# Kernel optimization log

Hardware: AMD Instinct MI355X
Metric: run time of the kernel (lower is better)

Reference implementation:

```python
import jax, jax.numpy as jnp
import numpy as np

B, T, H, V, S = 64, 32, 512, 32000, 400


def setup_inputs() -> dict:
    key = jax.random.key(0)
    ks = jax.random.split(key, 14)
    f = lambda k, s: jax.random.normal(k, s, dtype=jnp.float32)
    return {
        "inputs": jax.random.randint(ks[0], (B, T), 0, V),
        "embedding0": f(ks[1], (B, H)),
        "output0": f(ks[2], (B, H)),
        "tree_h0": f(ks[3], (B, H)),
        "tree_c0": f(ks[4], (B, H)),
        "tree_context": f(ks[5], (B, S, H)),
        "text_h0": f(ks[6], (B, H)),
        "text_c0": f(ks[7], (B, H)),
        "text_context": f(ks[8], (B, S, H)),
        "word_emb": f(ks[9], (V, H)) * 0.02,
        "Wx": f(ks[10], (2 * H, 4 * H)) * 0.02,   # LSTM input weights (input_size = 2H)
        "Wh": f(ks[11], (H, 4 * H)) * 0.02,       # LSTM recurrent weights
        "b": jnp.zeros((4 * H,), jnp.float32),
        "W_in": f(ks[12], (H, H)) * 0.02,         # attention score projection
        "W_out": f(ks[13], (4 * H, H)) * 0.02,    # attention combine projection
    }


def _lstm_cell(x, h, c, Wx, Wh, b):
    g = x @ Wx + h @ Wh + b                      # [B,4H]
    i, f, gg, o = jnp.split(g, 4, axis=-1)
    c_new = jax.nn.sigmoid(f) * c + jax.nn.sigmoid(i) * jnp.tanh(gg)
    h_new = jax.nn.sigmoid(o) * jnp.tanh(c_new)
    return h_new, c_new


def _attend(h, ctx, W_in):
    target = h @ W_in                             # [B,H]
    scores = jnp.einsum('bsh,bh->bs', ctx, target)
    attn = jax.nn.softmax(scores, axis=-1)
    return jnp.einsum('bs,bsh->bh', attn, ctx)    # weighted context [B,H]


def reference(inputs, embedding0, output0, tree_h0, tree_c0, tree_context,
              text_h0, text_c0, text_context, word_emb, Wx, Wh, b, W_in, W_out):
    embeddings = word_emb[inputs]                 # [B,T,H]
    embeddings = jnp.transpose(embeddings, (1, 0, 2))  # time-major [T,B,H]

    def step(carry, emb_i):
        emb, out, th, tc, xh, xc = carry
        x = jnp.concatenate([emb, out], axis=1)   # [B,2H]
        th, tc = _lstm_cell(x, th, tc, Wx, Wh, b)  # tree branch (shared weights)
        xh, xc = _lstm_cell(x, xh, xc, Wx, Wh, b)  # text branch (shared weights)
        w_tree = _attend(th, tree_context, W_in)
        w_text = _attend(xh, text_context, W_in)
        combined = jnp.concatenate([w_tree, w_text, th, xh], axis=1)  # [B,4H]
        out = jnp.tanh(combined @ W_out)           # dropout = identity (eval mode)
        return (emb_i, out, th, tc, xh, xc), out

    carry0 = (embedding0, output0, tree_h0, tree_c0, text_h0, text_c0)
    _, outs = jax.lax.scan(step, carry0, embeddings)  # outs: [T,B,H]
    return jnp.transpose(outs, (1, 0, 2))             # [B,T,H]
```

## Files before the change

### kernel.cpp

```cpp
#include <hip/hip_runtime.h>
#include <hip/hip_bf16.h>
#include <math.h>

#define BB 64
#define TT 32
#define HH 512
#define H2 1024
#define H4 2048
#define SS 400

#define OFF_WT_HI 0u
#define OFF_WT_LO 1572864u
#define OFF_WIT_HI 3145728u
#define OFF_WIT_LO 3276800u
#define OFF_EH    3407872u
#define OFF_EL    3932160u
#define OFF_OH    4456448u
#define OFF_OL    4472832u
#define OFF_HHP   4489216u
#define OFF_HLP   4521984u
#define OFF_TC    4554752u
#define OFF_XC    4620288u
#define OFF_TH    4685824u
#define OFF_XH    4751360u
#define OFF_G     4816896u
#define OFF_TGTP  6914048u
#define OFF_PACC  7438336u
#define OFF_PML   7962624u
#define OFF_CTX16 7964672u
#define WS_NEED_F 21071872u
#define OFF_WOT_HI 21071872u
#define OFF_WOT_LO 21596160u
#define OFF_COMBH  22120448u
#define OFF_COMBL  22153216u
#define WS_NEED2_F 22185984u
#define OFF_PART  OFF_G

typedef short bf16x8 __attribute__((ext_vector_type(8)));
typedef float f32x4  __attribute__((ext_vector_type(4)));

__device__ __forceinline__ float sigm(float x){ return 1.f/(1.f+__expf(-x)); }

__device__ __forceinline__ unsigned short bf_rn(float x){
  unsigned int u = __float_as_uint(x);
  return (unsigned short)((u + 0x7fffu + ((u>>16)&1u)) >> 16);
}
__device__ __forceinline__ void split2(float x, unsigned short &h, unsigned short &l){
  h = bf_rn(x);
  float hf = __uint_as_float(((unsigned int)h)<<16);
  l = bf_rn(x - hf);
}
__device__ __forceinline__ float blo(unsigned int u){ return __uint_as_float(u<<16); }
__device__ __forceinline__ float bhi(unsigned int u){ return __uint_as_float(u & 0xffff0000u); }

__global__ __launch_bounds__(256) void k_wprep(const float* __restrict__ Wx,
    const float* __restrict__ Wh, unsigned short* __restrict__ wt_hi,
    unsigned short* __restrict__ wt_lo){
  __shared__ float lds[64][68];
  int bk = blockIdx.x >> 5, bn = blockIdx.x & 31;
  int k0 = bk*64, n0 = bn*64;
  int tid = threadIdx.x;
  #pragma unroll
  for (int i=0;i<4;i++){
    int flat = tid + i*256;
    int k = flat >> 4, nq = flat & 15;
    int kg = k0 + k;
    const float* srow = (kg < 1024) ? Wx + (size_t)kg*H4 : Wh + (size_t)(kg-1024)*H4;
    float4 v = *(const float4*)(srow + n0 + nq*4);
    *(float4*)&lds[k][nq*4] = v;
  }
  __syncthreads();
  #pragma unroll
  for (int i=0;i<2;i++){
    int flat = tid + i*256;
    int n = flat >> 3, k8 = flat & 7;
    ushort4 h0, h1, l0, l1;
    unsigned short h[8], l[8];
    #pragma unroll
    for (int j=0;j<8;j++) split2(lds[k8*8+j][n], h[j], l[j]);
    h0.x=h[0];h0.y=h[1];h0.z=h[2];h0.w=h[3]; h1.x=h[4];h1.y=h[5];h1.z=h[6];h1.w=h[7];
    l0.x=l[0];l0.y=l[1];l0.z=l[2];l0.w=l[3]; l1.x=l[4];l1.y=l[5];l1.z=l[6];l1.w=l[7];
    size_t dst = (size_t)(n0+n)*1536 + k0 + k8*8;
    *(ushort4*)(wt_hi+dst) = h0; *(ushort4*)(wt_hi+dst+4) = h1;
    *(ushort4*)(wt_lo+dst) = l0; *(ushort4*)(wt_lo+dst+4) = l1;
  }
}

__global__ __launch_bounds__(256) void k_wiprep(const float* __restrict__ W_in,
    unsigned short* __restrict__ wit_hi, unsigned short* __restrict__ wit_lo){
  __shared__ float lds[64][68];
  int bk = blockIdx.x >> 3, bn = blockIdx.x & 7;
  int k0 = bk*64, n0 = bn*64;
  int tid = threadIdx.x;
  #pragma unroll
  for (int i=0;i<4;i++){
    int flat = tid + i*256;
    int k = flat >> 4, nq = flat & 15;
    float4 v = *(const float4*)(W_in + (size_t)(k0+k)*HH + n0 + nq*4);
    *(float4*)&lds[k][nq*4] = v;
  }
  __syncthreads();
  #pragma unroll
  for (int i=0;i<2;i++){
    int flat = tid + i*256;
    int n = flat >> 3, k8 = flat & 7;
    ushort4 h0, h1, l0, l1;
    unsigned short h[8], l[8];
    #pragma unroll
    for (int j=0;j<8;j++) split2(lds[k8*8+j][n], h[j], l[j]);
    h0.x=h[0];h0.y=h[1];h0.z=h[2];h0.w=h[3]; h1.x=h[4];h1.y=h[5];h1.z=h[6];h1.w=h[7];
    l0.x=l[0];l0.y=l[1];l0.z=l[2];l0.w=l[3]; l1.x=l[4];l1.y=l[5];l1.z=l[6];l1.w=l[7];
    size_t dst = (size_t)(n0+n)*HH + k0 + k8*8;
    *(ushort4*)(wit_hi+dst) = h0; *(ushort4*)(wit_hi+dst+4) = h1;
    *(ushort4*)(wit_lo+dst) = l0; *(ushort4*)(wit_lo+dst+4) = l1;
  }
}

__global__ __launch_bounds__(256) void k_woprep(const float* __restrict__ W_out,
    unsigned short* __restrict__ wot_hi, unsigned short* __restrict__ wot_lo){
  __shared__ float lds[64][68];
  int bk = blockIdx.x >> 3, bn = blockIdx.x & 7;
  int k0 = bk*64, n0 = bn*64;
  int tid = threadIdx.x;
  #pragma unroll
  for (int i=0;i<4;i++){
    int flat = tid + i*256;
    int k = flat >> 4, nq = flat & 15;
    float4 v = *(const float4*)(W_out + (size_t)(k0+k)*HH + n0 + nq*4);
    *(float4*)&lds[k][nq*4] = v;
  }
  __syncthreads();
  #pragma unroll
  for (int i=0;i<2;i++){
    int flat = tid + i*256;
    int n = flat >> 3, k8 = flat & 7;
    ushort4 h0, h1, l0, l1;
    unsigned short h[8], l[8];
    #pragma unroll
    for (int j=0;j<8;j++) split2(lds[k8*8+j][n], h[j], l[j]);
    h0.x=h[0];h0.y=h[1];h0.z=h[2];h0.w=h[3]; h1.x=h[4];h1.y=h[5];h1.z=h[6];h1.w=h[7];
    l0.x=l[0];l0.y=l[1];l0.z=l[2];l0.w=l[3]; l1.x=l[4];l1.y=l[5];l1.z=l[6];l1.w=l[7];
    size_t dst = (size_t)(n0+n)*H4 + k0 + k8*8;
    *(ushort4*)(wot_hi+dst) = h0; *(ushort4*)(wot_hi+dst+4) = h1;
    *(ushort4*)(wot_lo+dst) = l0; *(ushort4*)(wot_lo+dst+4) = l1;
  }
}

__global__ __launch_bounds__(256) void k_ctx16(const float* __restrict__ src,
    unsigned short* __restrict__ dst){
  size_t off = ((size_t)blockIdx.x*256 + threadIdx.x)*8;
  float4 a = *(const float4*)(src + off);
  float4 c = *(const float4*)(src + off + 4);
  ushort4 u0, u1;
  u0.x=bf_rn(a.x); u0.y=bf_rn(a.y); u0.z=bf_rn(a.z); u0.w=bf_rn(a.w);
  u1.x=bf_rn(c.x); u1.y=bf_rn(c.y); u1.z=bf_rn(c.z); u1.w=bf_rn(c.w);
  *(ushort4*)(dst+off) = u0;
  *(ushort4*)(dst+off+4) = u1;
}

__global__ __launch_bounds__(128) void k_prep(const int* __restrict__ inp,
    const float* __restrict__ emb0, const float* __restrict__ wemb,
    unsigned short* __restrict__ eh, unsigned short* __restrict__ el){
  int n = blockIdx.x; int t = n >> 6, b = n & 63;
  const float* src = (t==0) ? emb0 + (size_t)b*HH
                            : wemb + (size_t)inp[b*TT + (t-1)]*HH;
  float4 v = ((const float4*)src)[threadIdx.x];
  ushort4 h, l;
  split2(v.x,h.x,l.x); split2(v.y,h.y,l.y); split2(v.z,h.z,l.z); split2(v.w,h.w,l.w);
  size_t base = ((size_t)t*BB + b)*HH + threadIdx.x*4;
  *(ushort4*)(eh+base) = h; *(ushort4*)(el+base) = l;
}

__global__ __launch_bounds__(256) void k_init(const float* __restrict__ th0,
    const float* __restrict__ tc0, const float* __restrict__ xh0,
    const float* __restrict__ xc0, const float* __restrict__ out0,
    float* __restrict__ ws){
  unsigned short* hhp = (unsigned short*)(ws + OFF_HHP);
  unsigned short* hlp = (unsigned short*)(ws + OFF_HLP);
  unsigned short* oh  = (unsigned short*)(ws + OFF_OH);
  unsigned short* ol  = (unsigned short*)(ws + OFF_OL);
  int which = blockIdx.x >> 5;
  int idx = (blockIdx.x & 31)*256 + threadIdx.x;
  if (which==0){ ((float4*)(ws+OFF_TC))[idx] = ((const float4*)tc0)[idx]; return; }
  if (which==1){ ((float4*)(ws+OFF_XC))[idx] = ((const float4*)xc0)[idx]; return; }
  const float* s = which==2? th0 : which==3? xh0 : out0;
  float4 v = ((const float4*)s)[idx];
  ushort4 h, l;
  split2(v.x,h.x,l.x); split2(v.y,h.y,l.y); split2(v.z,h.z,l.z); split2(v.w,h.w,l.w);
  if (which==4){
    *(ushort4*)(oh + (size_t)idx*4) = h; *(ushort4*)(ol + (size_t)idx*4) = l;
  } else {
    size_t base = (size_t)(which-2)*BB*HH + (size_t)idx*4;
    *(ushort4*)(hhp+base) = h; *(ushort4*)(hlp+base) = l;
  }
}

__global__ __launch_bounds__(256) void k_gemm(const unsigned short* __restrict__ wt_hi,
    const unsigned short* __restrict__ wt_lo, const unsigned short* __restrict__ eh,
    const unsigned short* __restrict__ el, const unsigned short* __restrict__ oh,
    const unsigned short* __restrict__ ol, const unsigned short* __restrict__ hhp,
    const unsigned short* __restrict__ hlp, float* __restrict__ gpart, int t){
  int tid = threadIdx.x, lane = tid & 63, wave = tid >> 6;
  int bn = blockIdx.x & 31, ks = blockIdx.x >> 5;
  int lm = lane & 15, lk = (lane >> 4) << 3;
  f32x4 acc[2][4];
  #pragma unroll
  for (int i=0;i<2;i++)
    #pragma unroll
    for (int j=0;j<4;j++) acc[i][j] = (f32x4){0.f,0.f,0.f,0.f};
  size_t ebase[2], obase[2], hbase[2];
  #pragma unroll
  for (int i=0;i<2;i++){
    int r = (wave*2 + i)*16 + lm;
    int b = r & 63, br = r >> 6;
    ebase[i] = ((size_t)t*BB + b)*HH;
    obase[i] = (size_t)b*HH;
    hbase[i] = ((size_t)br*BB + b)*HH;
  }
  size_t wb[4];
  #pragma unroll
  for (int j=0;j<4;j++) wb[j] = (size_t)(bn*64 + j*16 + lm)*1536;
  #pragma unroll
  for (int c=0;c<6;c++){
    int kc = ks*192 + c*32;
    int sec = kc >> 9;
    int kk = (kc & 511) + lk;
    const unsigned short* ph = sec==0? eh : sec==1? oh : hhp;
    const unsigned short* pl = sec==0? el : sec==1? ol : hlp;
    bf16x8 ah[2], al[2], wh_[4], wl_[4];
    #pragma unroll
    for (int i=0;i<2;i++){
      size_t off = (sec==0? ebase[i] : sec==1? obase[i] : hbase[i]) + kk;
      ah[i] = *(const bf16x8*)(ph + off);
      al[i] = *(const bf16x8*)(pl + off);
    }
    int kw = kc + lk;
    #pragma unroll
    for (int j=0;j<4;j++){
      wh_[j] = *(const bf16x8*)(wt_hi + wb[j] + kw);
      wl_[j] = *(const bf16x8*)(wt_lo + wb[j] + kw);
    }
    #pragma unroll
    for (int i=0;i<2;i++)
      #pragma unroll
      for (int j=0;j<4;j++){
        acc[i][j] = __builtin_amdgcn_mfma_f32_16x16x32_bf16(ah[i], wh_[j], acc[i][j], 0,0,0);
        acc[i][j] = __builtin_amdgcn_mfma_f32_16x16x32_bf16(ah[i], wl_[j], acc[i][j], 0,0,0);
        acc[i][j] = __builtin_amdgcn_mfma_f32_16x16x32_bf16(al[i], wh_[j], acc[i][j], 0,0,0);
      }
  }
  int lr4 = (lane >> 4) * 4;
  #pragma unroll
  for (int i=0;i<2;i++){
    int m0 = (wave*2+i)*16;
    #pragma unroll
    for (int j=0;j<4;j++){
      int col = bn*64 + j*16 + lm;
      #pragma unroll
      for (int q=0;q<4;q++){
        int row = m0 + lr4 + q;
        gpart[((size_t)ks*128 + row)*H4 + col] = acc[i][j][q];
      }
    }
  }
}

__global__ __launch_bounds__(256) void k_lstm(float* __restrict__ ws,
    const float* __restrict__ bias, int rs){
  int gid = blockIdx.x*256 + threadIdx.x;
  int b = gid >> 9, j = gid & 511;
  int wsl = rs ^ 1;
  const float* gp = ws + OFF_G;
  unsigned short* hhp = (unsigned short*)(ws + OFF_HHP);
  unsigned short* hlp = (unsigned short*)(ws + OFF_HLP);
  #pragma unroll
  for (int br=0;br<2;br++){
    float g0=0.f,g1=0.f,g2=0.f,g3=0.f;
    #pragma unroll
    for (int ks=0;ks<8;ks++){
      size_t base = ((size_t)ks*128 + br*64 + b)*H4 + j;
      g0 += gp[base]; g1 += gp[base+512]; g2 += gp[base+1024]; g3 += gp[base+1536];
    }
    g0 += bias[j]; g1 += bias[512+j]; g2 += bias[1024+j]; g3 += bias[1536+j];
    size_t hoff = (br? OFF_XH : OFF_TH), coff = (br? OFF_XC : OFF_TC);
    float cold = ws[coff + (size_t)rs*BB*HH + (size_t)b*HH + j];
    float cn = sigm(g1)*cold + sigm(g0)*tanhf(g2);
    float hn = sigm(g3)*tanhf(cn);
    ws[coff + (size_t)wsl*BB*HH + (size_t)b*HH + j] = cn;
    ws[hoff + (size_t)wsl*BB*HH + (size_t)b*HH + j] = hn;
    unsigned short h_, l_;
    split2(hn, h_, l_);
    hhp[(size_t)(br*64+b)*HH + j] = h_;
    hlp[(size_t)(br*64+b)*HH + j] = l_;
  }
}

__global__ __launch_bounds__(256) void k_tgtB(const unsigned short* __restrict__ wit_hi,
    const unsigned short* __restrict__ wit_lo, const unsigned short* __restrict__ hhp,
    const unsigned short* __restrict__ hlp, float* __restrict__ tgt){
  int tid = threadIdx.x, lane = tid & 63, wave = tid >> 6;
  int cn = blockIdx.x & 7, mt = blockIdx.x >> 3;
  int lm = lane & 15, lk = (lane >> 4) << 3;
  f32x4 acc = (f32x4){0.f,0.f,0.f,0.f};
  size_t abase = (size_t)(mt*16 + lm)*HH;
  size_t wb = (size_t)(cn*64 + wave*16 + lm)*HH;
  #pragma unroll
  for (int c=0;c<16;c++){
    int kc = c*32 + lk;
    bf16x8 ah  = *(const bf16x8*)(hhp + abase + kc);
    bf16x8 al  = *(const bf16x8*)(hlp + abase + kc);
    bf16x8 wh_ = *(const bf16x8*)(wit_hi + wb + kc);
    bf16x8 wl_ = *(const bf16x8*)(wit_lo + wb + kc);
    acc = __builtin_amdgcn_mfma_f32_16x16x32_bf16(ah, wh_, acc, 0,0,0);
    acc = __builtin_amdgcn_mfma_f32_16x16x32_bf16(ah, wl_, acc, 0,0,0);
    acc = __builtin_amdgcn_mfma_f32_16x16x32_bf16(al, wh_, acc, 0,0,0);
  }
  int lr4 = (lane >> 4) * 4;
  int col = cn*64 + wave*16 + lm;
  #pragma unroll
  for (int q=0;q<4;q++)
    tgt[(size_t)(mt*16 + lr4 + q)*HH + col] = acc[q];
}

__global__ __launch_bounds__(512, 8) void k_attn(const float* __restrict__ tree_ctx,
    const float* __restrict__ text_ctx, const unsigned short* __restrict__ ctx16,
    float* __restrict__ ws, int use16){
  int blk = blockIdx.x;
  int sh = blk & 7, b = (blk>>3) & 63, branch = blk >> 9;
  int tid = threadIdx.x, lane = tid & 63, wave = tid >> 6;
  __shared__ float tgt_s[512];
  __shared__ float accs[8][512];
  __shared__ float wm_s[8], wl_s[8];
  int row128 = branch*64 + b;
  if (tid < 128)
    ((float4*)tgt_s)[tid] = ((const float4*)(ws + OFF_TGTP + (size_t)row128*HH))[tid];
  __syncthreads();
  const size_t CH = (size_t)BB*SS*HH;
  const float* ctxf = (branch? text_ctx : tree_ctx) + ((size_t)b*SS + sh*50)*HH;
  const unsigned short* c16 = ctx16 + (branch? CH:0) + ((size_t)b*SS + sh*50)*HH;
  float4 ta = *(const float4*)&tgt_s[lane*8];
  float4 tb = *(const float4*)&tgt_s[lane*8+4];
  float m = -INFINITY, l = 0.f;
  float a[8] = {0,0,0,0,0,0,0,0};
  if (use16){
    for (int r = wave; r < 50; r += 8){
      uint4 u = *(const uint4*)(c16 + (size_t)r*HH + lane*8);
      float v0=blo(u.x), v1=bhi(u.x), v2=blo(u.y), v3=bhi(u.y);
      float v4=blo(u.z), v5=bhi(u.z), v6=blo(u.w), v7=bhi(u.w);
      float p = v0*ta.x + v1*ta.y + v2*ta.z + v3*ta.w
              + v4*tb.x + v5*tb.y + v6*tb.z + v7*tb.w;
      #pragma unroll
      for (int off=32; off; off>>=1) p += __shfl_xor(p, off, 64);
      float mn = fmaxf(m, p);
      float scale = __expf(m - mn);
      float e = __expf(p - mn);
      l = l*scale + e;
      a[0] = a[0]*scale + e*v0; a[1] = a[1]*scale + e*v1;
      a[2] = a[2]*scale + e*v2; a[3] = a[3]*scale + e*v3;
      a[4] = a[4]*scale + e*v4; a[5] = a[5]*scale + e*v5;
      a[6] = a[6]*scale + e*v6; a[7] = a[7]*scale + e*v7;
      m = mn;
    }
  } else {
    for (int r = wave; r < 50; r += 8){
      const float* crow = ctxf + (size_t)r*HH + lane*8;
      float4 ca = *(const float4*)crow;
      float4 cb = *(const float4*)(crow+4);
      float p = ca.x*ta.x + ca.y*ta.y + ca.z*ta.z + ca.w*ta.w
              + cb.x*tb.x + cb.y*tb.y + cb.z*tb.z + cb.w*tb.w;
      #pragma unroll
      for (int off=32; off; off>>=1) p += __shfl_xor(p, off, 64);
      float mn = fmaxf(m, p);
      float scale = __expf(m - mn);
      float e = __expf(p - mn);
      l = l*scale + e;
      a[0] = a[0]*scale + e*ca.x; a[1] = a[1]*scale + e*ca.y;
      a[2] = a[2]*scale + e*ca.z; a[3] = a[3]*scale + e*ca.w;
      a[4] = a[4]*scale + e*cb.x; a[5] = a[5]*scale + e*cb.y;
      a[6] = a[6]*scale + e*cb.z; a[7] = a[7]*scale + e*cb.w;
      m = mn;
    }
  }
  if (lane==0){ wm_s[wave] = m; wl_s[wave] = l; }
  #pragma unroll
  for (int j=0;j<8;j++) accs[wave][lane*8+j] = a[j];
  __syncthreads();
  float M = wm_s[0];
  #pragma unroll
  for (int w8=1;w8<8;w8++) M = fmaxf(M, wm_s[w8]);
  float s = 0.f;
  #pragma unroll
  for (int w8=0;w8<8;w8++) s += accs[w8][tid] * __expf(wm_s[w8] - M);
  int pidx = (branch*64 + b)*8 + sh;
  ws[OFF_PACC + (size_t)pidx*HH + tid] = s;
  if (tid==0){
    float L = 0.f;
    #pragma unroll
    for (int w8=0;w8<8;w8++) L += wl_s[w8]*__expf(wm_s[w8] - M);
    ws[OFF_PML + (size_t)pidx*2]   = M;
    ws[OFF_PML + (size_t)pidx*2+1] = L;
  }
}

__global__ __launch_bounds__(256) void k_outA(float* __restrict__ ws){
  __shared__ float ce_s[2][8];
  int b = blockIdx.x, tid = threadIdx.x;
  if (tid < 2){
    int p0 = (tid*64 + b)*8;
    float mv[8], lv[8];
    float M = -INFINITY;
    #pragma unroll
    for (int i=0;i<8;i++){
      mv[i] = ws[OFF_PML + (size_t)(p0+i)*2];
      lv[i] = ws[OFF_PML + (size_t)(p0+i)*2+1];
      M = fmaxf(M, mv[i]);
    }
    float L = 0.f, ev[8];
    #pragma unroll
    for (int i=0;i<8;i++){ ev[i] = __expf(mv[i]-M); L += lv[i]*ev[i]; }
    #pragma unroll
    for (int i=0;i<8;i++) ce_s[tid][i] = ev[i]/L;
  }
  __syncthreads();
  int h = tid*4;
  int sec = h >> 9, hs = h & 511;
  int p0 = (sec*64 + b)*8;
  float4 v = {0,0,0,0};
  #pragma unroll
  for (int p=0;p<8;p++){
    float4 a = *(const float4*)(ws + OFF_PACC + (size_t)(p0+p)*HH + hs);
    float cw = ce_s[sec][p];
    v.x += a.x*cw; v.y += a.y*cw; v.z += a.z*cw; v.w += a.w*cw;
  }
  ushort4 hv, lv;
  split2(v.x,hv.x,lv.x); split2(v.y,hv.y,lv.y); split2(v.z,hv.z,lv.z); split2(v.w,hv.w,lv.w);
  unsigned short* ch = (unsigned short*)(ws + OFF_COMBH);
  unsigned short* cl = (unsigned short*)(ws + OFF_COMBL);
  *(ushort4*)(ch + (size_t)b*1024 + h) = hv;
  *(ushort4*)(cl + (size_t)b*1024 + h) = lv;
}

__global__ __launch_bounds__(256) void k_outBF(const unsigned short* __restrict__ wot_hi,
    const unsigned short* __restrict__ wot_lo, const unsigned short* __restrict__ combh,
    const unsigned short* __restrict__ combl, const unsigned short* __restrict__ hhp,
    const unsigned short* __restrict__ hlp, float* __restrict__ dout,
    unsigned short* __restrict__ oh, unsigned short* __restrict__ ol, int t){
  __shared__ float accs[4][16][17];
  int tid = threadIdx.x, lane = tid & 63, wave = tid >> 6;
  int nt = blockIdx.x & 31, mt = blockIdx.x >> 5;
  int lm = lane & 15, lk = (lane >> 4) << 3;
  f32x4 acc = (f32x4){0.f,0.f,0.f,0.f};
  int b = mt*16 + lm;
  int col = nt*16 + lm;
  size_t wb = (size_t)col*H4 + (size_t)wave*512;
  const unsigned short *pa_h, *pa_l;
  size_t abase;
  if (wave < 2){ pa_h = combh; pa_l = combl; abase = (size_t)b*1024 + (size_t)wave*512; }
  else         { pa_h = hhp;   pa_l = hlp;   abase = ((size_t)(wave-2)*64 + b)*HH; }
  #pragma unroll
  for (int c=0;c<16;c++){
    int kk = c*32 + lk;
    bf16x8 ah  = *(const bf16x8*)(pa_h + abase + kk);
    bf16x8 al  = *(const bf16x8*)(pa_l + abase + kk);
    bf16x8 wh_ = *(const bf16x8*)(wot_hi + wb + kk);
    bf16x8 wl_ = *(const bf16x8*)(wot_lo + wb + kk);
    acc = __builtin_amdgcn_mfma_f32_16x16x32_bf16(ah, wh_, acc, 0,0,0);
    acc = __builtin_amdgcn_mfma_f32_16x16x32_bf16(ah, wl_, acc, 0,0,0);
    acc = __builtin_amdgcn_mfma_f32_16x16x32_bf16(al, wh_, acc, 0,0,0);
  }
  int lr4 = (lane >> 4) * 4;
  #pragma unroll
  for (int q=0;q<4;q++) accs[wave][lr4+q][lm] = acc[q];
  __syncthreads();
  int row = tid >> 4, colL = tid & 15;
  float s = accs[0][row][colL] + accs[1][row][colL]
          + accs[2][row][colL] + accs[3][row][colL];
  float v = tanhf(s);
  int bb = mt*16 + row, cc = nt*16 + colL;
  dout[((size_t)bb*TT + t)*HH + cc] = v;
  unsigned short h_, l_;
  split2(v, h_, l_);
  oh[(size_t)bb*HH + cc] = h_;
  ol[(size_t)bb*HH + cc] = l_;
}

__global__ __launch_bounds__(256) void k_outB(const float* __restrict__ W_out,
    float* __restrict__ ws, int wsl){
  __shared__ float comb_s[16][256];
  __shared__ float ce_s[16][8];
  int tid = threadIdx.x, lane = tid & 63, wave = tid >> 6;
  int blk = blockIdx.x;
  int ct = blk & 7, bg = (blk>>3)&3, ks = blk>>5;
  int b0 = bg*16;
  int k0 = ks*256;
  int sec = ks >> 1;
  int kk0 = (ks & 1)*256;
  int c = ct*64 + lane;
  if (sec < 2){
    if (tid < 16){
      int b = b0 + tid;
      int p0 = (sec*64 + b)*8;
      float mv[8], lv[8];
      float M = -INFINITY;
      #pragma unroll
      for (int i=0;i<8;i++){
        mv[i] = ws[OFF_PML + (size_t)(p0+i)*2];
        lv[i] = ws[OFF_PML + (size_t)(p0+i)*2+1];
        M = fmaxf(M, mv[i]);
      }
      float L = 0.f, ev[8];
      #pragma unroll
      for (int i=0;i<8;i++){ ev[i] = __expf(mv[i]-M); L += lv[i]*ev[i]; }
      #pragma unroll
      for (int i=0;i<8;i++) ce_s[tid][i] = ev[i]/L;
    }
    __syncthreads();
  }
  #pragma unroll
  for (int i=0;i<4;i++){
    int flat = tid + i*256;
    int row = flat >> 6;
    int q   = flat & 63;
    int b = b0 + row;
    int h = kk0 + q*4;
    float4 v;
    if (sec < 2){
      int p0 = (sec*64 + b)*8;
      v.x = 0.f; v.y = 0.f; v.z = 0.f; v.w = 0.f;
      #pragma unroll
      for (int p=0;p<8;p++){
        float4 a = *(const float4*)(ws + OFF_PACC + (size_t)(p0+p)*HH + h);
        float cw = ce_s[row][p];
        v.x += a.x*cw; v.y += a.y*cw; v.z += a.z*cw; v.w += a.w*cw;
      }
    } else {
      size_t hoff = (sec==2 ? OFF_TH : OFF_XH) + (size_t)wsl*BB*HH;
      v = *(const float4*)(ws + hoff + (size_t)b*HH + h);
    }
    *(float4*)&comb_s[row][q*4] = v;
  }
  __syncthreads();
  float acc[4] = {0,0,0,0};
  #pragma unroll 4
  for (int k=0;k<256;k++){
    float wv = W_out[(size_t)(k0+k)*HH + c];
    #pragma unroll
    for (int i=0;i<4;i++) acc[i] += comb_s[wave*4+i][k]*wv;
  }
  #pragma unroll
  for (int i=0;i<4;i++){
    int b = b0 + wave*4 + i;
    ws[OFF_PART + ((size_t)ks*BB + b)*HH + c] = acc[i];
  }
}

__global__ __launch_bounds__(256) void k_outC(float* __restrict__ ws,
    float* __restrict__ dout, int t){
  int gid = blockIdx.x*256 + threadIdx.x;
  int b = gid >> 7, cq = gid & 127;
  int c0 = cq*4;
  float4 s = {0,0,0,0};
  #pragma unroll
  for (int ks=0;ks<8;ks++){
    float4 p = *(const float4*)(ws + OFF_PART + ((size_t)ks*BB + b)*HH + c0);
    s.x += p.x; s.y += p.y; s.z += p.z; s.w += p.w;
  }
  float4 o;
  o.x = tanhf(s.x); o.y = tanhf(s.y); o.z = tanhf(s.z); o.w = tanhf(s.w);
  *(float4*)(dout + ((size_t)b*TT + t)*HH + c0) = o;
  ushort4 h, l;
  split2(o.x,h.x,l.x); split2(o.y,h.y,l.y); split2(o.z,h.z,l.z); split2(o.w,h.w,l.w);
  unsigned short* oh = (unsigned short*)(ws + OFF_OH);
  unsigned short* ol = (unsigned short*)(ws + OFF_OL);
  *(ushort4*)(oh + (size_t)b*HH + c0) = h;
  *(ushort4*)(ol + (size_t)b*HH + c0) = l;
}

extern "C" void kernel_launch(void* const* d_in, const int* in_sizes, int n_in,
                              void* d_out, int out_size, void* d_ws, size_t ws_size,
                              hipStream_t stream){
  const int*   inp   = (const int*)  d_in[0];
  const float* emb0  = (const float*)d_in[1];
  const float* out0  = (const float*)d_in[2];
  const float* th0   = (const float*)d_in[3];
  const float* tc0   = (const float*)d_in[4];
  const float* trctx = (const float*)d_in[5];
  const float* xh0   = (const float*)d_in[6];
  const float* xc0   = (const float*)d_in[7];
  const float* txctx = (const float*)d_in[8];
  const float* wemb  = (const float*)d_in[9];
  const float* Wx    = (const float*)d_in[10];
  const float* Wh    = (const float*)d_in[11];
  const float* bias  = (const float*)d_in[12];
  const float* W_in  = (const float*)d_in[13];
  const float* W_out = (const float*)d_in[14];
  float* ws  = (float*)d_ws;
  float* out = (float*)d_out;
  unsigned short* wt_hi  = (unsigned short*)(ws + OFF_WT_HI);
  unsigned short* wt_lo  = (unsigned short*)(ws + OFF_WT_LO);
  unsigned short* wit_hi = (unsigned short*)(ws + OFF_WIT_HI);
  unsigned short* wit_lo = (unsigned short*)(ws + OFF_WIT_LO);
  unsigned short* wot_hi = (unsigned short*)(ws + OFF_WOT_HI);
  unsigned short* wot_lo = (unsigned short*)(ws + OFF_WOT_LO);
  unsigned short* combh  = (unsigned short*)(ws + OFF_COMBH);
  unsigned short* combl  = (unsigned short*)(ws + OFF_COMBL);
  unsigned short* eh  = (unsigned short*)(ws + OFF_EH);
  unsigned short* el  = (unsigned short*)(ws + OFF_EL);
  unsigned short* oh  = (unsigned short*)(ws + OFF_OH);
  unsigned short* ol  = (unsigned short*)(ws + OFF_OL);
  unsigned short* hhp = (unsigned short*)(ws + OFF_HHP);
  unsigned short* hlp = (unsigned short*)(ws + OFF_HLP);
  unsigned short* ctx16 = (unsigned short*)(ws + OFF_CTX16);
  float* gpart = ws + OFF_G;
  float* tgt   = ws + OFF_TGTP;
  int use16 = (ws_size >= (size_t)WS_NEED_F  * 4u) ? 1 : 0;
  int fast  = (ws_size >= (size_t)WS_NEED2_F * 4u) ? 1 : 0;
  const size_t CH = (size_t)BB*SS*HH;

  hipLaunchKernelGGL(k_wprep,  dim3(768),   dim3(256), 0, stream, Wx, Wh, wt_hi, wt_lo);
  hipLaunchKernelGGL(k_wiprep, dim3(64),    dim3(256), 0, stream, W_in, wit_hi, wit_lo);
  if (fast)
    hipLaunchKernelGGL(k_woprep, dim3(256), dim3(256), 0, stream, W_out, wot_hi, wot_lo);
  if (use16){
    hipLaunchKernelGGL(k_ctx16, dim3(6400), dim3(256), 0, stream, trctx, ctx16);
    hipLaunchKernelGGL(k_ctx16, dim3(6400), dim3(256), 0, stream, txctx, ctx16 + CH);
  }
  hipLaunchKernelGGL(k_prep,   dim3(TT*BB), dim3(128), 0, stream, inp, emb0, wemb, eh, el);
  hipLaunchKernelGGL(k_init,   dim3(160),   dim3(256), 0, stream, th0, tc0, xh0, xc0, out0, ws);
  for (int t=0; t<TT; t++){
    int rs = t & 1, wsl = rs ^ 1;
    hipLaunchKernelGGL(k_gemm, dim3(256),  dim3(256), 0, stream,
                       wt_hi, wt_lo, eh, el, oh, ol, hhp, hlp, gpart, t);
    hipLaunchKernelGGL(k_lstm, dim3(128),  dim3(256), 0, stream, ws, bias, rs);
    hipLaunchKernelGGL(k_tgtB, dim3(64),   dim3(256), 0, stream, wit_hi, wit_lo, hhp, hlp, tgt);
    hipLaunchKernelGGL(k_attn, dim3(1024), dim3(512), 0, stream, trctx, txctx, ctx16, ws, use16);
    if (fast){
      hipLaunchKernelGGL(k_outA,  dim3(64),  dim3(256), 0, stream, ws);
      hipLaunchKernelGGL(k_outBF, dim3(128), dim3(256), 0, stream,
                         wot_hi, wot_lo, combh, combl, hhp, hlp, out, oh, ol, t);
    } else {
      hipLaunchKernelGGL(k_outB, dim3(256), dim3(256), 0, stream, W_out, ws, wsl);
      hipLaunchKernelGGL(k_outC, dim3(32),  dim3(256), 0, stream, ws, out, t);
    }
  }
}
```

Before: 1.528 ms.

## Fuse LSTM gate GEMM with cell update and double-buffer hidden state

On the fast path, the split-K gate GEMM and the separate LSTM reduction kernel are replaced by one kernel. Each block computes all four gates for 16 rows by 16 hidden units, reduces the per-wave K partials in shared memory and applies the cell update in place. The bf16 hi/lo hidden state is now double-buffered by step parity, so the fused kernel can read the previous state while writing the new one. This removes one launch per step and the round trip of gate partials through global memory, at the cost of a narrower output tile per block and a 4-way K split inside the block. The fp32 h outputs (OFF_TH/OFF_XH) are no longer written on this path, so downstream kernels must not depend on them.

```diff
diff --git a/kernel.cpp b/kernel.cpp
--- a/kernel.cpp
+++ b/kernel.cpp
@@ -24,6 +24,8 @@
 #define OFF_TH    4685824u
 #define OFF_XH    4751360u
 #define OFF_G     4816896u
+#define OFF_HHP2  OFF_G
+#define OFF_HLP2  (OFF_G + 65536u)
 #define OFF_TGTP  6914048u
 #define OFF_PACC  7438336u
 #define OFF_PML   7962624u
@@ -174,9 +176,8 @@
 __global__ __launch_bounds__(256) void k_init(const float* __restrict__ th0,
     const float* __restrict__ tc0, const float* __restrict__ xh0,
     const float* __restrict__ xc0, const float* __restrict__ out0,
-    float* __restrict__ ws){
-  unsigned short* hhp = (unsigned short*)(ws + OFF_HHP);
-  unsigned short* hlp = (unsigned short*)(ws + OFF_HLP);
+    float* __restrict__ ws, unsigned short* __restrict__ hp,
+    unsigned short* __restrict__ lp){
   unsigned short* oh  = (unsigned short*)(ws + OFF_OH);
   unsigned short* ol  = (unsigned short*)(ws + OFF_OL);
   int which = blockIdx.x >> 5;
@@ -191,108 +192,75 @@
     *(ushort4*)(oh + (size_t)idx*4) = h; *(ushort4*)(ol + (size_t)idx*4) = l;
   } else {
     size_t base = (size_t)(which-2)*BB*HH + (size_t)idx*4;
-    *(ushort4*)(hhp+base) = h; *(ushort4*)(hlp+base) = l;
-  }
-}
-
-__global__ __launch_bounds__(256) void k_gemm(const unsigned short* __restrict__ wt_hi,
+    *(ushort4*)(hp+base) = h; *(ushort4*)(lp+base) = l;
+  }
+}
+
+__global__ __launch_bounds__(256) void k_gemmL(const unsigned short* __restrict__ wt_hi,
     const unsigned short* __restrict__ wt_lo, const unsigned short* __restrict__ eh,
     const unsigned short* __restrict__ el, const unsigned short* __restrict__ oh,
-    const unsigned short* __restrict__ ol, const unsigned short* __restrict__ hhp,
-    const unsigned short* __restrict__ hlp, float* __restrict__ gpart, int t){
+    const unsigned short* __restrict__ ol, unsigned short* __restrict__ hhp2,
+    unsigned short* __restrict__ hlp2, float* __restrict__ ws,
+    const float* __restrict__ bias, int t, int rs){
+  __shared__ float accs[4][4][16][17];
   int tid = threadIdx.x, lane = tid & 63, wave = tid >> 6;
-  int bn = blockIdx.x & 31, ks = blockIdx.x >> 5;
+  int jt = blockIdx.x & 31, mt = blockIdx.x >> 5;
   int lm = lane & 15, lk = (lane >> 4) << 3;
-  f32x4 acc[2][4];
-  #pragma unroll
-  for (int i=0;i<2;i++)
-    #pragma unroll
-    for (int j=0;j<4;j++) acc[i][j] = (f32x4){0.f,0.f,0.f,0.f};
-  size_t ebase[2], obase[2], hbase[2];
-  #pragma unroll
-  for (int i=0;i<2;i++){
-    int r = (wave*2 + i)*16 + lm;
-    int b = r & 63, br = r >> 6;
-    ebase[i] = ((size_t)t*BB + b)*HH;
-    obase[i] = (size_t)b*HH;
-    hbase[i] = ((size_t)br*BB + b)*HH;
-  }
+  int wsl = rs ^ 1;
+  f32x4 acc[4];
+  #pragma unroll
+  for (int g=0;g<4;g++) acc[g] = (f32x4){0.f,0.f,0.f,0.f};
+  int r = mt*16 + lm;
+  size_t ebase = ((size_t)t*BB + (r & 63))*HH;
+  size_t obase = (size_t)(r & 63)*HH;
+  size_t hbase = ((size_t)rs*128 + r)*HH;
   size_t wb[4];
   #pragma unroll
-  for (int j=0;j<4;j++) wb[j] = (size_t)(bn*64 + j*16 + lm)*1536;
-  #pragma unroll
-  for (int c=0;c<6;c++){
-    int kc = ks*192 + c*32;
-    int sec = kc >> 9;
-    int kk = (kc & 511) + lk;
-    const unsigned short* ph = sec==0? eh : sec==1? oh : hhp;
-    const unsigned short* pl = sec==0? el : sec==1? ol : hlp;
-    bf16x8 ah[2], al[2], wh_[4], wl_[4];
-    #pragma unroll
-    for (int i=0;i<2;i++){
-      size_t off = (sec==0? ebase[i] : sec==1? obase[i] : hbase[i]) + kk;
-      ah[i] = *(const bf16x8*)(ph + off);
-      al[i] = *(const bf16x8*)(pl + off);
-    }
-    int kw = kc + lk;
-    #pragma unroll
-    for (int j=0;j<4;j++){
-      wh_[j] = *(const bf16x8*)(wt_hi + wb[j] + kw);
-      wl_[j] = *(const bf16x8*)(wt_lo + wb[j] + kw);
-    }
-    #pragma unroll
-    for (int i=0;i<2;i++)
-      #pragma unroll
-      for (int j=0;j<4;j++){
-        acc[i][j] = __builtin_amdgcn_mfma_f32_16x16x32_bf16(ah[i], wh_[j], acc[i][j], 0,0,0);
-        acc[i][j] = __builtin_amdgcn_mfma_f32_16x16x32_bf16(ah[i], wl_[j], acc[i][j], 0,0,0);
-        acc[i][j] = __builtin_amdgcn_mfma_f32_16x16x32_bf16(al[i], wh_[j], acc[i][j], 0,0,0);
-      }
+  for (int g=0;g<4;g++) wb[g] = (size_t)(g*512 + jt*16 + lm)*1536;
+  #pragma unroll
+  for (int c=0;c<12;c++){
+    int kg = wave*384 + c*32;
+    int sec = kg >> 9;
+    int kk = (kg & 511) + lk;
+    bf16x8 ah, al;
+    if (sec==0){ ah = *(const bf16x8*)(eh + ebase + kk); al = *(const bf16x8*)(el + ebase + kk); }
+    else if (sec==1){ ah = *(const bf16x8*)(oh + obase + kk); al = *(const bf16x8*)(ol + obase + kk); }
+    else { ah = *(const bf16x8*)(hhp2 + hbase + kk); al = *(const bf16x8*)(hlp2 + hbase + kk); }
+    int kw = kg + lk;
+    #pragma unroll
+    for (int g=0;g<4;g++){
+      bf16x8 wh_ = *(const bf16x8*)(wt_hi + wb[g] + kw);
+      bf16x8 wl_ = *(const bf16x8*)(wt_lo + wb[g] + kw);
+      acc[g] = __builtin_amdgcn_mfma_f32_16x16x32_bf16(ah, wh_, acc[g], 0,0,0);
+      acc[g] = __builtin_amdgcn_mfma_f32_16x16x32_bf16(ah, wl_, acc[g], 0,0,0);
+      acc[g] = __builtin_amdgcn_mfma_f32_16x16x32_bf16(al, wh_, acc[g], 0,0,0);
+    }
   }
   int lr4 = (lane >> 4) * 4;
   #pragma unroll
-  for (int i=0;i<2;i++){
-    int m0 = (wave*2+i)*16;
-    #pragma unroll
-    for (int j=0;j<4;j++){
-      int col = bn*64 + j*16 + lm;
-      #pragma unroll
-      for (int q=0;q<4;q++){
-        int row = m0 + lr4 + q;
-        gpart[((size_t)ks*128 + row)*H4 + col] = acc[i][j][q];
-      }
-    }
-  }
-}
-
-__global__ __launch_bounds__(256) void k_lstm(float* __restrict__ ws,
-    const float* __restrict__ bias, int rs){
-  int gid = blockIdx.x*256 + threadIdx.x;
-  int b = gid >> 9, j = gid & 511;
-  int wsl = rs ^ 1;
-  const float* gp = ws + OFF_G;
-  unsigned short* hhp = (unsigned short*)(ws + OFF_HHP);
-  unsigned short* hlp = (unsigned short*)(ws + OFF_HLP);
-  #pragma unroll
-  for (int br=0;br<2;br++){
-    float g0=0.f,g1=0.f,g2=0.f,g3=0.f;
-    #pragma unroll
-    for (int ks=0;ks<8;ks++){
-      size_t base = ((size_t)ks*128 + br*64 + b)*H4 + j;
-      g0 += gp[base]; g1 += gp[base+512]; g2 += gp[base+1024]; g3 += gp[base+1536];
-    }
-    g0 += bias[j]; g1 += bias[512+j]; g2 += bias[1024+j]; g3 += bias[1536+j];
-    size_t hoff = (br? OFF_XH : OFF_TH), coff = (br? OFF_XC : OFF_TC);
-    float cold = ws[coff + (size_t)rs*BB*HH + (size_t)b*HH + j];
-    float cn = sigm(g1)*cold + sigm(g0)*tanhf(g2);
-    float hn = sigm(g3)*tanhf(cn);
-    ws[coff + (size_t)wsl*BB*HH + (size_t)b*HH + j] = cn;
-    ws[hoff + (size_t)wsl*BB*HH + (size_t)b*HH + j] = hn;
-    unsigned short h_, l_;
-    split2(hn, h_, l_);
-    hhp[(size_t)(br*64+b)*HH + j] = h_;
-    hlp[(size_t)(br*64+b)*HH + j] = l_;
-  }
+  for (int g=0;g<4;g++)
+    #pragma unroll
+    for (int q=0;q<4;q++)
+      accs[wave][g][lr4+q][lm] = acc[g][q];
+  __syncthreads();
+  int row = tid >> 4, jl = tid & 15;
+  int jglob = jt*16 + jl;
+  int rr = mt*16 + row;
+  int br = rr >> 6, b = rr & 63;
+  float g4[4];
+  #pragma unroll
+  for (int gi=0;gi<4;gi++)
+    g4[gi] = accs[0][gi][row][jl] + accs[1][gi][row][jl]
+           + accs[2][gi][row][jl] + accs[3][gi][row][jl] + bias[gi*512 + jglob];
+  size_t coff = br ? OFF_XC : OFF_TC;
+  float cold = ws[coff + (size_t)rs*BB*HH + (size_t)b*HH + jglob];
+  float cn = sigm(g4[1])*cold + sigm(g4[0])*tanhf(g4[2]);
+  float hn = sigm(g4[3])*tanhf(cn);
+  ws[coff + (size_t)wsl*BB*HH + (size_t)b*HH + jglob] = cn;
+  unsigned short h_, l_;
+  split2(hn, h_, l_);
+  size_t hidx = ((size_t)wsl*128 + rr)*HH + jglob;
+  hhp2[hidx] = h_; hlp2[hidx] = l_;
 }
 
 __global__ __launch_bounds__(256) void k_tgtB(const unsigned short* __restrict__ wit_hi,
@@ -482,6 +450,106 @@
   split2(v, h_, l_);
   oh[(size_t)bb*HH + cc] = h_;
   ol[(size_t)bb*HH + cc] = l_;
+}
+
+__global__ __launch_bounds__(256) void k_gemm(const unsigned short* __restrict__ wt_hi,
+    const unsigned short* __restrict__ wt_lo, const unsigned short* __restrict__ eh,
+    const unsigned short* __restrict__ el, const unsigned short* __restrict__ oh,
+    const unsigned short* __restrict__ ol, const unsigned short* __restrict__ hhp,
+    const unsigned short* __restrict__ hlp, float* __restrict__ gpart, int t){
+  int tid = threadIdx.x, lane = tid & 63, wave = tid >> 6;
+  int bn = blockIdx.x & 31, ks = blockIdx.x >> 5;
+  int lm = lane & 15, lk = (lane >> 4) << 3;
+  f32x4 acc[2][4];
+  #pragma unroll
+  for (int i=0;i<2;i++)
+    #pragma unroll
+    for (int j=0;j<4;j++) acc[i][j] = (f32x4){0.f,0.f,0.f,0.f};
+  size_t ebase[2], obase[2], hbase[2];
+  #pragma unroll
+  for (int i=0;i<2;i++){
+    int r = (wave*2 + i)*16 + lm;
+    int b = r & 63, br = r >> 6;
+    ebase[i] = ((size_t)t*BB + b)*HH;
+    obase[i] = (size_t)b*HH;
+    hbase[i] = ((size_t)br*BB + b)*HH;
+  }
+  size_t wb[4];
+  #pragma unroll
+  for (int j=0;j<4;j++) wb[j] = (size_t)(bn*64 + j*16 + lm)*1536;
+  #pragma unroll
+  for (int c=0;c<6;c++){
+    int kc = ks*192 + c*32;
+    int sec = kc >> 9;
+    int kk = (kc & 511) + lk;
+    const unsigned short* ph = sec==0? eh : sec==1? oh : hhp;
+    const unsigned short* pl = sec==0? el : sec==1? ol : hlp;
+    bf16x8 ah[2], al[2], wh_[4], wl_[4];
+    #pragma unroll
+    for (int i=0;i<2;i++){
+      size_t off = (sec==0? ebase[i] : sec==1? obase[i] : hbase[i]) + kk;
+      ah[i] = *(const bf16x8*)(ph + off);
+      al[i] = *(const bf16x8*)(pl + off);
+    }
+    int kw = kc + lk;
+    #pragma unroll
+    for (int j=0;j<4;j++){
+      wh_[j] = *(const bf16x8*)(wt_hi + wb[j] + kw);
+      wl_[j] = *(const bf16x8*)(wt_lo + wb[j] + kw);
+    }
+    #pragma unroll
+    for (int i=0;i<2;i++)
+      #pragma unroll
+      for (int j=0;j<4;j++){
+        acc[i][j] = __builtin_amdgcn_mfma_f32_16x16x32_bf16(ah[i], wh_[j], acc[i][j], 0,0,0);
+        acc[i][j] = __builtin_amdgcn_mfma_f32_16x16x32_bf16(ah[i], wl_[j], acc[i][j], 0,0,0);
+        acc[i][j] = __builtin_amdgcn_mfma_f32_16x16x32_bf16(al[i], wh_[j], acc[i][j], 0,0,0);
+      }
+  }
+  int lr4 = (lane >> 4) * 4;
+  #pragma unroll
+  for (int i=0;i<2;i++){
+    int m0 = (wave*2+i)*16;
+    #pragma unroll
+    for (int j=0;j<4;j++){
+      int col = bn*64 + j*16 + lm;
+      #pragma unroll
+      for (int q=0;q<4;q++){
+        int row = m0 + lr4 + q;
+        gpart[((size_t)ks*128 + row)*H4 + col] = acc[i][j][q];
+      }
+    }
+  }
+}
+
+__global__ __launch_bounds__(256) void k_lstm(float* __restrict__ ws,
+    const float* __restrict__ bias, int rs){
+  int gid = blockIdx.x*256 + threadIdx.x;
+  int b = gid >> 9, j = gid & 511;
+  int wsl = rs ^ 1;
+  const float* gp = ws + OFF_G;
+  unsigned short* hhp = (unsigned short*)(ws + OFF_HHP);
+  unsigned short* hlp = (unsigned short*)(ws + OFF_HLP);
+  #pragma unroll
+  for (int br=0;br<2;br++){
+    float g0=0.f,g1=0.f,g2=0.f,g3=0.f;
+    #pragma unroll
+    for (int ks=0;ks<8;ks++){
+      size_t base = ((size_t)ks*128 + br*64 + b)*H4 + j;
+      g0 += gp[base]; g1 += gp[base+512]; g2 += gp[base+1024]; g3 += gp[base+1536];
+    }
+    g0 += bias[j]; g1 += bias[512+j]; g2 += bias[1024+j]; g3 += bias[1536+j];
+    size_t hoff = (br? OFF_XH : OFF_TH), coff = (br? OFF_XC : OFF_TC);
+    float cold = ws[coff + (size_t)rs*BB*HH + (size_t)b*HH + j];
+    float cn = sigm(g1)*cold + sigm(g0)*tanhf(g2);
+    float hn = sigm(g3)*tanhf(cn);
+    ws[coff + (size_t)wsl*BB*HH + (size_t)b*HH + j] = cn;
+    ws[hoff + (size_t)wsl*BB*HH + (size_t)b*HH + j] = hn;
+    unsigned short h_, l_;
+    split2(hn, h_, l_);
+    hhp[(size_t)(br*64+b)*HH + j] = h_;
+    hlp[(size_t)(br*64+b)*HH + j] = l_;
+  }
 }
 
 __global__ __launch_bounds__(256) void k_outB(const float* __restrict__ W_out,
@@ -610,6 +678,8 @@
   unsigned short* ol  = (unsigned short*)(ws + OFF_OL);
   unsigned short* hhp = (unsigned short*)(ws + OFF_HHP);
   unsigned short* hlp = (unsigned short*)(ws + OFF_HLP);
+  unsigned short* hhp2 = (unsigned short*)(ws + OFF_HHP2);
+  unsigned short* hlp2 = (unsigned short*)(ws + OFF_HLP2);
   unsigned short* ctx16 = (unsigned short*)(ws + OFF_CTX16);
   float* gpart = ws + OFF_G;
   float* tgt   = ws + OFF_TGTP;
@@ -626,19 +696,26 @@
     hipLaunchKernelGGL(k_ctx16, dim3(6400), dim3(256), 0, stream, txctx, ctx16 + CH);
   }
   hipLaunchKernelGGL(k_prep,   dim3(TT*BB), dim3(128), 0, stream, inp, emb0, wemb, eh, el);
-  hipLaunchKernelGGL(k_init,   dim3(160),   dim3(256), 0, stream, th0, tc0, xh0, xc0, out0, ws);
+  hipLaunchKernelGGL(k_init,   dim3(160),   dim3(256), 0, stream, th0, tc0, xh0, xc0, out0,
+                     ws, fast? hhp2 : hhp, fast? hlp2 : hlp);
   for (int t=0; t<TT; t++){
     int rs = t & 1, wsl = rs ^ 1;
-    hipLaunchKernelGGL(k_gemm, dim3(256),  dim3(256), 0, stream,
-                       wt_hi, wt_lo, eh, el, oh, ol, hhp, hlp, gpart, t);
-    hipLaunchKernelGGL(k_lstm, dim3(128),  dim3(256), 0, stream, ws, bias, rs);
-    hipLaunchKernelGGL(k_tgtB, dim3(64),   dim3(256), 0, stream, wit_hi, wit_lo, hhp, hlp, tgt);
-    hipLaunchKernelGGL(k_attn, dim3(1024), dim3(512), 0, stream, trctx, txctx, ctx16, ws, use16);
     if (fast){
-      hipLaunchKernelGGL(k_outA,  dim3(64),  dim3(256), 0, stream, ws);
+      unsigned short* hh_w = hhp2 + (size_t)wsl*128*HH;
+      unsigned short* hl_w = hlp2 + (size_t)wsl*128*HH;
+      hipLaunchKernelGGL(k_gemmL, dim3(256), dim3(256), 0, stream,
+                         wt_hi, wt_lo, eh, el, oh, ol, hhp2, hlp2, ws, bias, t, rs);
+      hipLaunchKernelGGL(k_tgtB, dim3(64), dim3(256), 0, stream, wit_hi, wit_lo, hh_w, hl_w, tgt);
+      hipLaunchKernelGGL(k_attn, dim3(1024), dim3(512), 0, stream, trctx, txctx, ctx16, ws, use16);
+      hipLaunchKernelGGL(k_outA, dim3(64), dim3(256), 0, stream, ws);
       hipLaunchKernelGGL(k_outBF, dim3(128), dim3(256), 0, stream,
-                         wot_hi, wot_lo, combh, combl, hhp, hlp, out, oh, ol, t);
+                         wot_hi, wot_lo, combh, combl, hh_w, hl_w, out, oh, ol, t);
     } else {
+      hipLaunchKernelGGL(k_gemm, dim3(256), dim3(256), 0, stream,
+                         wt_hi, wt_lo, eh, el, oh, ol, hhp, hlp, gpart, t);
+      hipLaunchKernelGGL(k_lstm, dim3(128), dim3(256), 0, stream, ws, bias, rs);
+      hipLaunchKernelGGL(k_tgtB, dim3(64),  dim3(256), 0, stream, wit_hi, wit_lo, hhp, hlp, tgt);
+      hipLaunchKernelGGL(k_attn, dim3(1024), dim3(512), 0, stream, trctx, txctx, ctx16, ws, use16);
       hipLaunchKernelGGL(k_outB, dim3(256), dim3(256), 0, stream, W_out, ws, wsl);
       hipLaunchKernelGGL(k_outC, dim3(32),  dim3(256), 0, stream, ws, out, t);
     }
```

Result: slower. 1.646 ms (+7.7%).
